# Performance work log

Measured on AMD Instinct MI355X. Metric: run time of the kernel, lower is better.

## Reference

```python
import jax, jax.numpy as jnp
import numpy as np
from jax import lax

B, T, S, D = 16, 16, 196, 768
H = 256          # hidden_dim
NH = 4           # attention heads
TH = 32          # temporal hidden = max(16, H//8)
UP = 4           # UPSAMPLE_FACTOR


def _ln(x, w, b):
    m = jnp.mean(x, -1, keepdims=True)
    v = jnp.mean((x - m) ** 2, -1, keepdims=True)
    return (x - m) / jnp.sqrt(v + 1e-5) * w + b


def _gelu(x):
    return jax.nn.gelu(x, approximate=False)  # torch nn.GELU default (erf)


def _upmat(g, f):
    # torch F.interpolate bilinear, align_corners=False, as a [g*f, g] matrix
    g_up = g * f
    src = np.maximum((np.arange(g_up) + 0.5) / f - 0.5, 0.0)
    i0 = np.minimum(np.floor(src).astype(np.int64), g - 1)
    i1 = np.minimum(i0 + 1, g - 1)
    w1 = (src - i0).astype(np.float32)
    w0 = 1.0 - w1
    W = np.zeros((g_up, g), dtype=np.float32)
    np.add.at(W, (np.arange(g_up), i0), w0)
    np.add.at(W, (np.arange(g_up), i1), w1)
    return jnp.asarray(W)


def setup_inputs() -> dict:
    key = jax.random.key(0)
    ks = jax.random.split(key, 12)
    r = lambda i, shape: jax.random.normal(ks[i], shape, jnp.float32) * 0.02
    return dict(
        tokens=jax.random.normal(ks[0], (B, T * S, D), jnp.float32),
        num_frames=T,
        fixed_box_wh=jax.random.uniform(ks[1], (2,), jnp.float32, 0.1, 0.5),
        ln_w=jnp.ones((D,), jnp.float32), ln_b=jnp.zeros((D,), jnp.float32),
        query=r(2, (1, 1, D)),
        in_proj_w=r(3, (3 * D, D)), in_proj_b=jnp.zeros((3 * D,), jnp.float32),
        out_w=r(4, (D, D)), out_b=jnp.zeros((D,), jnp.float32),
        an_w=jnp.ones((D,), jnp.float32), an_b=jnp.zeros((D,), jnp.float32),
        obj_w=r(5, (1, D)), obj_b=jnp.zeros((1,), jnp.float32),
        temperature=jnp.asarray(8.0, jnp.float32),
        r1_w=r(6, (H, 2 * D)), r1_b=jnp.zeros((H,), jnp.float32),
        r2_w=r(7, (H // 2, H)), r2_b=jnp.zeros((H // 2,), jnp.float32),
        r3_w=r(8, (2, H // 2)), r3_b=jnp.zeros((2,), jnp.float32),
        tc1_w=r(9, (TH, 2, 5)), tc1_b=jnp.zeros((TH,), jnp.float32),
        tc2_w=r(10, (2, TH, 5)), tc2_b=jnp.zeros((2,), jnp.float32),
    )


def reference(tokens, num_frames, fixed_box_wh, ln_w, ln_b, query,
              in_proj_w, in_proj_b, out_w, out_b, an_w, an_b, obj_w, obj_b,
              temperature, r1_w, r1_b, r2_w, r2_b, r3_w, r3_b,
              tc1_w, tc1_b, tc2_w, tc2_b):
    Bb, N, Dd = tokens.shape
    Tt = int(num_frames)
    Ss = N // Tt
    g = int(round(Ss ** 0.5))
    g_up = g * UP
    BT = Bb * Tt
    dt = tokens.dtype

    normed = _ln(tokens, ln_w, ln_b)
    flat = normed.reshape(BT, Ss, Dd)  # per-frame tokens

    # --- attention pooling with learned query (dropout off, eval) ---
    Wq, Wk, Wv = jnp.split(in_proj_w, 3, 0)
    bq, bk, bv = jnp.split(in_proj_b, 3, 0)
    dh = Dd // NH
    qh = (query.reshape(1, Dd) @ Wq.T + bq).reshape(NH, dh)  # same query for all frames
    kh = (flat @ Wk.T + bk).reshape(BT, Ss, NH, dh)
    vh = (flat @ Wv.T + bv).reshape(BT, Ss, NH, dh)
    scores = jnp.einsum('hd,bshd->bhs', qh, kh) / jnp.sqrt(jnp.asarray(dh, dt))
    attnp = jax.nn.softmax(scores, -1)
    ctx = jnp.einsum('bhs,bshd->bhd', attnp, vh).reshape(BT, Dd)
    pooled = _ln(ctx @ out_w.T + out_b, an_w, an_b)

    obj = (flat @ obj_w.T + obj_b)[..., 0]  # [BT,S]
    Wu = _upmat(g, UP)
    up = jnp.einsum('ug,bgh,vh->buv', Wu, obj.reshape(BT, g, g), Wu)
    up = up.reshape(BT, g_up * g_up)
    temp = jnp.maximum(temperature, 1.0)
    probs = jax.nn.softmax(up * temp, -1)
    coords = (jnp.arange(g_up, dtype=dt) + 0.5) / g_up
    yy, xx = jnp.meshgrid(coords, coords, indexing='ij')
    cx0 = probs @ xx.reshape(-1)
    cy0 = probs @ yy.reshape(-1)

    # --- 3x3 local token gather around coarse center ---
    cxg = jnp.clip(cx0 * g, 0, g - 1).astype(jnp.int32)
    cyg = jnp.clip(cy0 * g, 0, g - 1).astype(jnp.int32)
    off = jnp.array([-1, 0, 1], jnp.int32)
    gy = jnp.clip(cyg[:, None, None] + off[None, :, None], 0, g - 1)
    gx = jnp.clip(cxg[:, None, None] + off[None, None, :], 0, g - 1)
    idx = (gy * g + gx).reshape(BT, 9)
    local = jnp.take_along_axis(flat, idx[:, :, None], axis=1).mean(1)

    # --- refine MLP ---
    h1 = _gelu(jnp.concatenate([pooled, local], -1) @ r1_w.T + r1_b)
    h2 = _gelu(h1 @ r2_w.T + r2_b)
    delta = h2 @ r3_w.T + r3_b
    cx = jnp.clip(cx0 + 0.3 * jnp.tanh(delta[:, 0]), 0.0, 1.0)
    cy = jnp.clip(cy0 + 0.3 * jnp.tanh(delta[:, 1]), 0.0, 1.0)

    # --- temporal residual refiner over center trajectories ---
    seq = jnp.stack([cx, cy], 1).reshape(Bb, Tt, 2).transpose(0, 2, 1)  # [B,2,T]
    dn = ('NCH', 'OIH', 'NCH')
    t1 = _gelu(lax.conv_general_dilated(seq, tc1_w, (1,), [(2, 2)],
                                        dimension_numbers=dn) + tc1_b[None, :, None])
    td = lax.conv_general_dilated(t1, tc2_w, (1,), [(2, 2)],
                                  dimension_numbers=dn) + tc2_b[None, :, None]
    td = td.transpose(0, 2, 1).reshape(BT, 2)
    cx = jnp.clip(cx + 0.12 * jnp.tanh(td[:, 0]), 0.0, 1.0)
    cy = jnp.clip(cy + 0.12 * jnp.tanh(td[:, 1]), 0.0, 1.0)

    # --- fixed-size boxes ---
    min_size = 1.0 / g
    wh = jnp.clip(jnp.broadcast_to(fixed_box_wh.reshape(1, 2), (Bb, 2)), min_size, 1.0)
    wh = jnp.broadcast_to(wh[:, None, :], (Bb, Tt, 2)).reshape(BT, 2)
    w, h = wh[:, 0], wh[:, 1]
    x1 = jnp.clip(cx - 0.5 * w, 0.0, 1.0)
    y1 = jnp.clip(cy - 0.5 * h, 0.0, 1.0)
    x2 = jnp.clip(cx + 0.5 * w, 0.0, 1.0)
    y2 = jnp.clip(cy + 0.5 * h, 0.0, 1.0)
    x2 = jnp.clip(jnp.maximum(x2, x1 + min_size), 0.0, 1.0)
    y2 = jnp.clip(jnp.maximum(y2, y1 + min_size), 0.0, 1.0)
    return jnp.stack([x1, y1, x2, y2], 1).reshape(Bb, Tt, 4)
```

## Files before the change

kernel.cpp:

```cpp
#include <hip/hip_runtime.h>
#include <hip/hip_bf16.h>
#include <math.h>

#define SS 196
#define DD 768

__device__ __forceinline__ float b2f(ushort u){
  union { unsigned int i; float f; } v; v.i = ((unsigned int)u) << 16; return v.f;
}
__device__ __forceinline__ bool bfmode(const void* lnw){
  return ((const ushort*)lnw)[0] != 0;
}
__device__ __forceinline__ float ldx(const void* p, size_t i, bool bf){
  return bf ? b2f(((const ushort*)p)[i]) : ((const float*)p)[i];
}
__device__ __forceinline__ float gelu_f(float x){
  return 0.5f * x * (1.0f + erff(x * 0.70710678118654752f));
}
__device__ __forceinline__ float wredsum(float v){
  #pragma unroll
  for(int o=32;o;o>>=1) v += __shfl_xor(v,o,64);
  return v;
}
__device__ __forceinline__ float wredmax(float v){
  #pragma unroll
  for(int o=32;o;o>>=1) v = fmaxf(v, __shfl_xor(v,o,64));
  return v;
}

__global__ __launch_bounds__(256) void k_qh(const void* __restrict__ q,
                                            const void* __restrict__ wq,
                                            const void* __restrict__ bq,
                                            const void* __restrict__ flagp,
                                            float* __restrict__ qh){
  bool bf = bfmode(flagp);
  int wv = threadIdx.x >> 6, lane = threadIdx.x & 63;
  int c = blockIdx.x * 4 + wv;
  float acc = 0.f;
  #pragma unroll
  for(int i=0;i<12;i++){ int d = lane + 64*i; acc += ldx(q,d,bf) * ldx(wq,(size_t)c*DD+d,bf); }
  acc = wredsum(acc);
  if(lane==0) qh[c] = acc + ldx(bq,c,bf);
}

__global__ __launch_bounds__(256) void k_wkeff(const void* __restrict__ wproj,
                                               const float* __restrict__ qh,
                                               const void* __restrict__ lnw,
                                               const void* __restrict__ objw,
                                               float* __restrict__ wkraw,
                                               float* __restrict__ wf){
  bool bf = bfmode(lnw);
  int idx = blockIdx.x*256 + threadIdx.x;
  int h = idx / DD, d = idx - h*DD;
  size_t base = ((size_t)(DD + h*192))*DD + d;
  const float* qp = qh + h*192;
  float acc = 0.f;
  #pragma unroll 8
  for(int j=0;j<192;j++) acc += qp[j] * ldx(wproj, base + (size_t)j*DD, bf);
  wkraw[idx] = acc;
  float w = ldx(lnw,d,bf);
  wf[idx] = w * acc;
  if(h==0) wf[4*DD + d] = w * ldx(objw,d,bf);
}

__global__ __launch_bounds__(256) void k_consts(const float* __restrict__ wf,
                                                const float* __restrict__ wkraw,
                                                const void* __restrict__ lnb,
                                                const void* __restrict__ objw,
                                                const void* __restrict__ flagp,
                                                float* __restrict__ s12){
  bool bf = bfmode(flagp);
  int wv = threadIdx.x >> 6, lane = threadIdx.x & 63;
  for(int r = wv; r < 10; r += 4){
    float acc = 0.f;
    #pragma unroll
    for(int i=0;i<12;i++){
      int d = lane + 64*i;
      if(r < 5)      acc += wf[r*DD + d];
      else if(r < 9) acc += ldx(lnb,d,bf) * wkraw[(r-5)*DD + d];
      else           acc += ldx(lnb,d,bf) * ldx(objw,d,bf);
    }
    acc = wredsum(acc);
    if(lane==0) s12[r] = acc;
  }
}

__global__ __launch_bounds__(256) void k_pass1(const void* __restrict__ tok,
                                               const float* __restrict__ wf,
                                               const float* __restrict__ s12,
                                               const void* __restrict__ objb,
                                               const void* __restrict__ flagp,
                                               float* __restrict__ scores,
                                               float* __restrict__ objv,
                                               float* __restrict__ meanv,
                                               float* __restrict__ rstdv){
  __shared__ __align__(16) float swf[5*DD];
  __shared__ float ss12[10];
  for(int i=threadIdx.x;i<5*DD;i+=256) swf[i]=wf[i];
  if(threadIdx.x<10) ss12[threadIdx.x]=s12[threadIdx.x];
  __syncthreads();
  bool bf = bfmode(flagp);
  int wv = threadIdx.x >> 6, lane = threadIdx.x & 63;
  for(int it=0; it<4; it++){
    int tkn = blockIdx.x*16 + wv*4 + it;
    int f = tkn / SS, s = tkn - f*SS;
    float a0=0,a1=0,a2=0,a3=0,a4=0,sm=0,sq=0;
    if(bf){
      const ushort* x = (const ushort*)tok + (size_t)tkn * DD;
      #pragma unroll
      for(int i=0;i<6;i++){
        int d = 2*lane + 128*i;
        ushort2 u = *(const ushort2*)(x + d);
        float x0=b2f(u.x), x1=b2f(u.y);
        sm += x0 + x1; sq += x0*x0 + x1*x1;
        float2 w;
        w = *(const float2*)&swf[0*DD+d]; a0 += x0*w.x + x1*w.y;
        w = *(const float2*)&swf[1*DD+d]; a1 += x0*w.x + x1*w.y;
        w = *(const float2*)&swf[2*DD+d]; a2 += x0*w.x + x1*w.y;
        w = *(const float2*)&swf[3*DD+d]; a3 += x0*w.x + x1*w.y;
        w = *(const float2*)&swf[4*DD+d]; a4 += x0*w.x + x1*w.y;
      }
    } else {
      const float* x = (const float*)tok + (size_t)tkn * DD;
      #pragma unroll
      for(int i=0;i<3;i++){
        int d = 4*lane + 256*i;
        float4 u = *(const float4*)(x + d);
        sm += u.x+u.y+u.z+u.w;
        sq += u.x*u.x+u.y*u.y+u.z*u.z+u.w*u.w;
        float4 w;
        w = *(const float4*)&swf[0*DD+d]; a0 += u.x*w.x+u.y*w.y+u.z*w.z+u.w*w.w;
        w = *(const float4*)&swf[1*DD+d]; a1 += u.x*w.x+u.y*w.y+u.z*w.z+u.w*w.w;
        w = *(const float4*)&swf[2*DD+d]; a2 += u.x*w.x+u.y*w.y+u.z*w.z+u.w*w.w;
        w = *(const float4*)&swf[3*DD+d]; a3 += u.x*w.x+u.y*w.y+u.z*w.z+u.w*w.w;
        w = *(const float4*)&swf[4*DD+d]; a4 += u.x*w.x+u.y*w.y+u.z*w.z+u.w*w.w;
      }
    }
    sm=wredsum(sm); sq=wredsum(sq);
    a0=wredsum(a0); a1=wredsum(a1); a2=wredsum(a2); a3=wredsum(a3); a4=wredsum(a4);
    if(lane==0){
      const float invD = 1.0f/768.0f;
      float m = sm*invD;
      float var = sq*invD - m*m;
      float rstd = rsqrtf(var + 1e-5f);
      meanv[tkn]=m; rstdv[tkn]=rstd;
      const float sc = 0.07216878364870322f;
      scores[(f*4+0)*SS+s] = (rstd*(a0 - m*ss12[0]) + ss12[5]) * sc;
      scores[(f*4+1)*SS+s] = (rstd*(a1 - m*ss12[1]) + ss12[6]) * sc;
      scores[(f*4+2)*SS+s] = (rstd*(a2 - m*ss12[2]) + ss12[7]) * sc;
      scores[(f*4+3)*SS+s] = (rstd*(a3 - m*ss12[3]) + ss12[8]) * sc;
      objv[tkn] = rstd*(a4 - m*ss12[4]) + ss12[9] + ldx(objb,0,bf);
    }
  }
}

__global__ __launch_bounds__(256) void k_soft(const float* __restrict__ rstdv,
                                              const float* __restrict__ meanv,
                                              float* __restrict__ scores,
                                              float* __restrict__ cterm){
  int f = blockIdx.x;
  int h = threadIdx.x >> 6, lane = threadIdx.x & 63;
  float* sc = scores + (size_t)(f*4+h)*SS;
  const float* rs = rstdv + f*SS;
  const float* mv = meanv + f*SS;
  float v[4]; float mx = -1e30f;
  #pragma unroll
  for(int j=0;j<4;j++){ int s=lane+64*j; v[j] = (s<SS)? sc[s] : -1e30f; mx=fmaxf(mx,v[j]); }
  mx = wredmax(mx);
  float e[4], sum=0.f;
  #pragma unroll
  for(int j=0;j<4;j++){ int s=lane+64*j; e[j] = (s<SS)? expf(v[j]-mx) : 0.f; sum += e[j]; }
  sum = wredsum(sum);
  float inv = 1.0f/sum;
  float cp = 0.f;
  #pragma unroll
  for(int j=0;j<4;j++){
    int s=lane+64*j;
    if(s<SS){ float r=rs[s]; float a=e[j]*inv*r; sc[s]=a; cp += a*mv[s]; }
  }
  cp = wredsum(cp);
  if(lane==0) cterm[f*4+h] = cp;
}

__global__ __launch_bounds__(256) void k_xbar(const void* __restrict__ tok,
                                              const float* __restrict__ aw,
                                              const float* __restrict__ cterm,
                                              const void* __restrict__ lnw,
                                              const void* __restrict__ lnb,
                                              float* __restrict__ xbar){
  bool bf = bfmode(lnw);
  int f = blockIdx.x;
  __shared__ float a4[SS*4];
  for(int i=threadIdx.x;i<SS*4;i+=256){ int s=i>>2, h=i&3; a4[i]=aw[(size_t)(f*4+h)*SS+s]; }
  __syncthreads();
  float acc[3][4] = {};
  if(bf){
    const ushort* tf = (const ushort*)tok + (size_t)f*SS*DD;
    for(int s=0;s<SS;s++){
      float w0=a4[s*4+0], w1=a4[s*4+1], w2=a4[s*4+2], w3=a4[s*4+3];
      #pragma unroll
      for(int j=0;j<3;j++){
        float x = b2f(tf[(size_t)s*DD + threadIdx.x + 256*j]);
        acc[j][0]+=w0*x; acc[j][1]+=w1*x; acc[j][2]+=w2*x; acc[j][3]+=w3*x;
      }
    }
  } else {
    const float* tf = (const float*)tok + (size_t)f*SS*DD;
    for(int s=0;s<SS;s++){
      float w0=a4[s*4+0], w1=a4[s*4+1], w2=a4[s*4+2], w3=a4[s*4+3];
      #pragma unroll
      for(int j=0;j<3;j++){
        float x = tf[(size_t)s*DD + threadIdx.x + 256*j];
        acc[j][0]+=w0*x; acc[j][1]+=w1*x; acc[j][2]+=w2*x; acc[j][3]+=w3*x;
      }
    }
  }
  float c0=cterm[f*4+0], c1=cterm[f*4+1], c2=cterm[f*4+2], c3=cterm[f*4+3];
  #pragma unroll
  for(int j=0;j<3;j++){
    int d = threadIdx.x + 256*j;
    float w=ldx(lnw,d,bf), b=ldx(lnb,d,bf);
    xbar[((size_t)(f*4+0))*DD+d] = w*(acc[j][0]-c0)+b;
    xbar[((size_t)(f*4+1))*DD+d] = w*(acc[j][1]-c1)+b;
    xbar[((size_t)(f*4+2))*DD+d] = w*(acc[j][2]-c2)+b;
    xbar[((size_t)(f*4+3))*DD+d] = w*(acc[j][3]-c3)+b;
  }
}

template<int N, int K, int ACT, int CTX, int ROWOFF>
__global__ __launch_bounds__(256) void k_gemm(const float* __restrict__ A,
                                              const void* __restrict__ W,
                                              const void* __restrict__ bias,
                                              const void* __restrict__ flagp,
                                              float* __restrict__ C){
  bool bf = bfmode(flagp);
  __shared__ float As[16][32];
  __shared__ float Bs[16][64];
  int tid = threadIdx.x;
  int m0 = blockIdx.y * 32;
  int n0 = blockIdx.x * 64;
  int h  = n0 / 192;
  int am = tid >> 3;
  int ak = (tid & 7) * 2;
  int bn = tid >> 2;
  int bk = (tid & 3) * 4;
  const size_t arow = CTX ? ((size_t)(m0+am)*4 + h) * 768 : (size_t)(m0+am) * K;
  const float* arp  = A + arow + ak;
  const size_t woff = (size_t)(ROWOFF + n0 + bn)*K + bk;
  int ry = tid >> 4;
  int cx = tid & 15;
  float acc[2][4] = {};
  for(int k0=0; k0<K; k0+=16){
    float2 av = *(const float2*)(arp + k0);
    float4 wv4;
    if(bf){
      ushort4 wv = *(const ushort4*)((const ushort*)W + woff + k0);
      wv4.x=b2f(wv.x); wv4.y=b2f(wv.y); wv4.z=b2f(wv.z); wv4.w=b2f(wv.w);
    } else {
      wv4 = *(const float4*)((const float*)W + woff + k0);
    }
    __syncthreads();
    As[ak][am]   = av.x;
    As[ak+1][am] = av.y;
    Bs[bk][bn]   = wv4.x;
    Bs[bk+1][bn] = wv4.y;
    Bs[bk+2][bn] = wv4.z;
    Bs[bk+3][bn] = wv4.w;
    __syncthreads();
    #pragma unroll
    for(int k=0;k<16;k++){
      float a0 = As[k][ry*2], a1 = As[k][ry*2+1];
      float4 b = *(const float4*)&Bs[k][cx*4];
      acc[0][0]+=a0*b.x; acc[0][1]+=a0*b.y; acc[0][2]+=a0*b.z; acc[0][3]+=a0*b.w;
      acc[1][0]+=a1*b.x; acc[1][1]+=a1*b.y; acc[1][2]+=a1*b.z; acc[1][3]+=a1*b.w;
    }
  }
  int n = n0 + cx*4;
  float b0=ldx(bias,ROWOFF+n,bf), b1=ldx(bias,ROWOFF+n+1,bf),
        b2v=ldx(bias,ROWOFF+n+2,bf), b3=ldx(bias,ROWOFF+n+3,bf);
  #pragma unroll
  for(int i=0;i<2;i++){
    int f = m0 + ry*2 + i;
    float4 o;
    o.x = acc[i][0]+b0; o.y = acc[i][1]+b1; o.z = acc[i][2]+b2v; o.w = acc[i][3]+b3;
    if(ACT==1){ o.x=gelu_f(o.x); o.y=gelu_f(o.y); o.z=gelu_f(o.z); o.w=gelu_f(o.w); }
    *(float4*)&C[(size_t)f*N + n] = o;
  }
}

__global__ __launch_bounds__(256) void k_lnan(const float* __restrict__ X,
                                              const void* __restrict__ anw,
                                              const void* __restrict__ anb,
                                              const void* __restrict__ flagp,
                                              float* __restrict__ pl){
  bool bf = bfmode(flagp);
  int wv = threadIdx.x >> 6, lane = threadIdx.x & 63;
  int f = blockIdx.x*4 + wv;
  const float* x = X + (size_t)f*DD;
  float v[12]; float sm=0, sq=0;
  #pragma unroll
  for(int i=0;i<12;i++){ v[i]=x[lane+64*i]; sm+=v[i]; sq+=v[i]*v[i]; }
  sm=wredsum(sm); sq=wredsum(sq);
  float m = sm*(1.0f/768.0f);
  float rstd = rsqrtf(sq*(1.0f/768.0f) - m*m + 1e-5f);
  #pragma unroll
  for(int i=0;i<12;i++){
    int d = lane+64*i;
    pl[(size_t)f*1536 + d] = (v[i]-m)*rstd*ldx(anw,d,bf) + ldx(anb,d,bf);
  }
}

__global__ __launch_bounds__(256) void k_obj(const void* __restrict__ tok,
                                             const float* __restrict__ objv,
                                             const float* __restrict__ meanv,
                                             const float* __restrict__ rstdv,
                                             const void* __restrict__ temp,
                                             const void* __restrict__ lnw,
                                             const void* __restrict__ lnb,
                                             float* __restrict__ pl,
                                             float* __restrict__ cxy){
  bool bf = bfmode(lnw);
  int f = blockIdx.x;
  int tid = threadIdx.x;
  __shared__ float G[196];
  __shared__ float up[3136];
  __shared__ int   i0a[56], i1a[56];
  __shared__ float w0a[56], w1a[56];
  __shared__ float redm[4], reds[4], redx[4], redy[4];
  __shared__ int   sidx[9];
  __shared__ float rj[9], rmj[9];
  if(tid<196) G[tid] = objv[(size_t)f*SS + tid];
  if(tid<56){
    float src = fmaxf((tid+0.5f)*0.25f - 0.5f, 0.0f);
    int i0 = min((int)floorf(src), 13);
    i0a[tid]=i0; i1a[tid]=min(i0+1,13);
    float w1 = src - (float)i0;
    w1a[tid]=w1; w0a[tid]=1.0f-w1;
  }
  __syncthreads();
  float lmax = -1e30f;
  for(int i=tid;i<3136;i+=256){
    int u=i/56, v=i-u*56;
    float val = w0a[u]*(w0a[v]*G[i0a[u]*14+i0a[v]] + w1a[v]*G[i0a[u]*14+i1a[v]])
              + w1a[u]*(w0a[v]*G[i1a[u]*14+i0a[v]] + w1a[v]*G[i1a[u]*14+i1a[v]]);
    up[i]=val; lmax=fmaxf(lmax,val);
  }
  lmax = wredmax(lmax);
  if((tid&63)==0) redm[tid>>6]=lmax;
  __syncthreads();
  float mx = fmaxf(fmaxf(redm[0],redm[1]), fmaxf(redm[2],redm[3]));
  float t = fmaxf(ldx(temp,0,bf), 1.0f);
  float se=0, sx=0, sy=0;
  for(int i=tid;i<3136;i+=256){
    int u=i/56, v=i-u*56;
    float e = expf((up[i]-mx)*t);
    se += e;
    sx += e * ((v+0.5f)*(1.0f/56.0f));
    sy += e * ((u+0.5f)*(1.0f/56.0f));
  }
  se=wredsum(se); sx=wredsum(sx); sy=wredsum(sy);
  if((tid&63)==0){ reds[tid>>6]=se; redx[tid>>6]=sx; redy[tid>>6]=sy; }
  __syncthreads();
  se = reds[0]+reds[1]+reds[2]+reds[3];
  sx = redx[0]+redx[1]+redx[2]+redx[3];
  sy = redy[0]+redy[1]+redy[2]+redy[3];
  float cx0 = sx/se, cy0 = sy/se;
  if(tid==0){ cxy[f*2]=cx0; cxy[f*2+1]=cy0; }
  float vx = fminf(fmaxf(cx0*14.0f,0.0f),13.0f); int cxg=(int)vx;
  float vy = fminf(fmaxf(cy0*14.0f,0.0f),13.0f); int cyg=(int)vy;
  if(tid<9){
    int dy = tid/3 - 1, dx = tid%3 - 1;
    int gy = min(max(cyg+dy,0),13), gx = min(max(cxg+dx,0),13);
    int s = gy*14+gx;
    sidx[tid]=s;
    float r = rstdv[(size_t)f*SS+s];
    rj[tid]=r; rmj[tid]=r*meanv[(size_t)f*SS+s];
  }
  __syncthreads();
  float offc = 0.f;
  #pragma unroll
  for(int j=0;j<9;j++) offc += rmj[j];
  for(int d=tid; d<DD; d+=256){
    float acc = 0.f;
    #pragma unroll
    for(int j=0;j<9;j++) acc += rj[j]*ldx(tok, (size_t)f*SS*DD + (size_t)sidx[j]*DD + d, bf);
    pl[(size_t)f*1536 + DD + d] = ldx(lnw,d,bf)*((acc-offc)*(1.0f/9.0f)) + ldx(lnb,d,bf);
  }
}

__global__ __launch_bounds__(256) void k_final(const float* __restrict__ h2,
                                               const void* __restrict__ r3w,
                                               const void* __restrict__ r3b,
                                               const float* __restrict__ cxy,
                                               const void* __restrict__ tc1w,
                                               const void* __restrict__ tc1b,
                                               const void* __restrict__ tc2w,
                                               const void* __restrict__ tc2b,
                                               const void* __restrict__ fbw,
                                               const void* __restrict__ flagp,
                                               void* __restrict__ out){
  bool bf = bfmode(flagp);
  __shared__ float sxs[256], sys[256];
  __shared__ float t1[16*32*16];
  __shared__ float td[16*2*16];
  int f = threadIdx.x;
  float a0=0.f, a1=0.f;
  const float* hh = h2 + (size_t)f*128;
  for(int k=0;k<128;k++){ float x=hh[k]; a0 += x*ldx(r3w,k,bf); a1 += x*ldx(r3w,128+k,bf); }
  a0 += ldx(r3b,0,bf); a1 += ldx(r3b,1,bf);
  float cx1 = fminf(fmaxf(cxy[f*2]   + 0.3f*tanhf(a0), 0.f), 1.f);
  float cy1 = fminf(fmaxf(cxy[f*2+1] + 0.3f*tanhf(a1), 0.f), 1.f);
  sxs[f]=cx1; sys[f]=cy1;
  __syncthreads();
  for(int idx=f; idx<8192; idx+=256){
    int b = idx>>9, o = (idx>>4)&31, t = idx&15;
    float acc = ldx(tc1b,o,bf);
    #pragma unroll
    for(int k=0;k<5;k++){
      int tt = t + k - 2;
      if(tt>=0 && tt<16)
        acc += sxs[b*16+tt]*ldx(tc1w,o*10 + k,bf) + sys[b*16+tt]*ldx(tc1w,o*10 + 5 + k,bf);
    }
    t1[idx] = gelu_f(acc);
  }
  __syncthreads();
  for(int idx=f; idx<512; idx+=256){
    int b = idx>>5, c = (idx>>4)&1, t = idx&15;
    float acc = ldx(tc2b,c,bf);
    for(int o=0;o<32;o++){
      #pragma unroll
      for(int k=0;k<5;k++){
        int tt = t + k - 2;
        if(tt>=0 && tt<16) acc += t1[(b*32+o)*16+tt]*ldx(tc2w,(c*32+o)*5+k,bf);
      }
    }
    td[(b*2+c)*16+t] = acc;
  }
  __syncthreads();
  {
    int t = f&15; (void)t;
    int b = f>>4;
    float tdx = td[(b*2+0)*16+(f&15)], tdy = td[(b*2+1)*16+(f&15)];
    float cx2 = fminf(fmaxf(sxs[f] + 0.12f*tanhf(tdx), 0.f), 1.f);
    float cy2 = fminf(fmaxf(sys[f] + 0.12f*tanhf(tdy), 0.f), 1.f);
    const float ms = 1.0f/14.0f;
    float w  = fminf(fmaxf(ldx(fbw,0,bf), ms), 1.f);
    float ht = fminf(fmaxf(ldx(fbw,1,bf), ms), 1.f);
    float x1 = fminf(fmaxf(cx2 - 0.5f*w , 0.f), 1.f);
    float y1 = fminf(fmaxf(cy2 - 0.5f*ht, 0.f), 1.f);
    float x2 = fminf(fmaxf(cx2 + 0.5f*w , 0.f), 1.f);
    float y2 = fminf(fmaxf(cy2 + 0.5f*ht, 0.f), 1.f);
    x2 = fminf(fmaxf(fmaxf(x2, x1+ms), 0.f), 1.f);
    y2 = fminf(fmaxf(fmaxf(y2, y1+ms), 0.f), 1.f);
    if(bf){
      __hip_bfloat16* ob = (__hip_bfloat16*)out;
      ob[f*4+0]=__float2bfloat16(x1);
      ob[f*4+1]=__float2bfloat16(y1);
      ob[f*4+2]=__float2bfloat16(x2);
      ob[f*4+3]=__float2bfloat16(y2);
    } else {
      float* of = (float*)out;
      of[f*4+0]=x1; of[f*4+1]=y1; of[f*4+2]=x2; of[f*4+3]=y2;
    }
  }
}

extern "C" void kernel_launch(void* const* d_in, const int* in_sizes, int n_in,
                              void* d_out, int out_size, void* d_ws, size_t ws_size,
                              hipStream_t stream){
  (void)in_sizes; (void)n_in; (void)out_size; (void)ws_size;
  const void* tok   = d_in[0];
  const void* fbw   = d_in[2];
  const void* lnw   = d_in[3];
  const void* lnb   = d_in[4];
  const void* query = d_in[5];
  const void* wproj = d_in[6];
  const void* bproj = d_in[7];
  const void* outw  = d_in[8];
  const void* outb  = d_in[9];
  const void* anw   = d_in[10];
  const void* anb   = d_in[11];
  const void* objw  = d_in[12];
  const void* objb  = d_in[13];
  const void* temp  = d_in[14];
  const void* r1w   = d_in[15];
  const void* r1b   = d_in[16];
  const void* r2w   = d_in[17];
  const void* r2b   = d_in[18];
  const void* r3w   = d_in[19];
  const void* r3b   = d_in[20];
  const void* tc1w  = d_in[21];
  const void* tc1b  = d_in[22];
  const void* tc2w  = d_in[23];
  const void* tc2b  = d_in[24];

  float* ws    = (float*)d_ws;
  float* qh    = ws;
  float* wkraw = ws + 768;
  float* wf    = wkraw + 3072;
  float* s12   = wf + 3840;
  float* scores= s12 + 16;
  float* objv  = scores + 200704;
  float* meanv = objv + 50176;
  float* rstdv = meanv + 50176;
  float* cterm = rstdv + 50176;
  float* xbar  = cterm + 1024;
  float* ctx   = xbar + 786432;
  float* ppre  = ctx + 196608;
  float* pl    = ppre + 196608;
  float* h1    = pl + 393216;
  float* h2    = h1 + 65536;
  float* cxy   = h2 + 32768;

  hipLaunchKernelGGL(k_qh,    dim3(192),  dim3(256), 0, stream, query, wproj, bproj, lnw, qh);
  hipLaunchKernelGGL(k_wkeff, dim3(12),   dim3(256), 0, stream, wproj, qh, lnw, objw, wkraw, wf);
  hipLaunchKernelGGL(k_consts,dim3(1),    dim3(256), 0, stream, wf, wkraw, lnb, objw, lnw, s12);
  hipLaunchKernelGGL(k_pass1, dim3(3136), dim3(256), 0, stream, tok, wf, s12, objb, lnw, scores, objv, meanv, rstdv);
  hipLaunchKernelGGL(k_soft,  dim3(256),  dim3(256), 0, stream, rstdv, meanv, scores, cterm);
  hipLaunchKernelGGL(k_xbar,  dim3(256),  dim3(256), 0, stream, tok, scores, cterm, lnw, lnb, xbar);
  hipLaunchKernelGGL((k_gemm<768,768,0,1,1536>), dim3(12,8), dim3(256), 0, stream, xbar, wproj, bproj, lnw, ctx);
  hipLaunchKernelGGL((k_gemm<768,768,0,0,0>),    dim3(12,8), dim3(256), 0, stream, ctx, outw, outb, lnw, ppre);
  hipLaunchKernelGGL(k_lnan,  dim3(64),   dim3(256), 0, stream, ppre, anw, anb, lnw, pl);
  hipLaunchKernelGGL(k_obj,   dim3(256),  dim3(256), 0, stream, tok, objv, meanv, rstdv, temp, lnw, lnb, pl, cxy);
  hipLaunchKernelGGL((k_gemm<256,1536,1,0,0>), dim3(4,8), dim3(256), 0, stream, pl, r1w, r1b, lnw, h1);
  hipLaunchKernelGGL((k_gemm<128,256,1,0,0>),  dim3(2,8), dim3(256), 0, stream, h1, r2w, r2b, lnw, h2);
  hipLaunchKernelGGL(k_final, dim3(1),    dim3(256), 0, stream, h2, r3w, r3b, cxy, tc1w, tc1b, tc2w, tc2b, fbw, lnw, (void*)d_out);
}
```

Before: 616.7 us.

## Replace shared-memory tiled GEMM with per-thread dot-product GEMM over more blocks

Swaps the LDS-tiled 32x64 GEMM for a kernel where each thread computes one output as a direct dot product over K, reading A rows and W rows with vector loads. The grid grows from 8 to 64 row-blocks, with 4 rows per block, so the small GEMMs (M=256) spread across many more CUs. This removes shared memory and barriers but drops operand reuse. Each thread streams a separate W row, so lanes access strided addresses and loads are uncoalesced, which adds memory traffic.

```diff
diff --git a/kernel.cpp b/kernel.cpp
--- a/kernel.cpp
+++ b/kernel.cpp
@@ -228,64 +228,45 @@
 }
 
 template<int N, int K, int ACT, int CTX, int ROWOFF>
-__global__ __launch_bounds__(256) void k_gemm(const float* __restrict__ A,
-                                              const void* __restrict__ W,
-                                              const void* __restrict__ bias,
-                                              const void* __restrict__ flagp,
-                                              float* __restrict__ C){
+__global__ __launch_bounds__(256) void k_dgemm(const float* __restrict__ A,
+                                               const void* __restrict__ W,
+                                               const void* __restrict__ bias,
+                                               const void* __restrict__ flagp,
+                                               float* __restrict__ C){
   bool bf = bfmode(flagp);
-  __shared__ float As[16][32];
-  __shared__ float Bs[16][64];
   int tid = threadIdx.x;
-  int m0 = blockIdx.y * 32;
-  int n0 = blockIdx.x * 64;
+  int m0 = blockIdx.y*4, n0 = blockIdx.x*64;
+  int mi = tid >> 6;
+  int n  = n0 + (tid & 63);
   int h  = n0 / 192;
-  int am = tid >> 3;
-  int ak = (tid & 7) * 2;
-  int bn = tid >> 2;
-  int bk = (tid & 3) * 4;
-  const size_t arow = CTX ? ((size_t)(m0+am)*4 + h) * 768 : (size_t)(m0+am) * K;
-  const float* arp  = A + arow + ak;
-  const size_t woff = (size_t)(ROWOFF + n0 + bn)*K + bk;
-  int ry = tid >> 4;
-  int cx = tid & 15;
-  float acc[2][4] = {};
-  for(int k0=0; k0<K; k0+=16){
-    float2 av = *(const float2*)(arp + k0);
-    float4 wv4;
-    if(bf){
-      ushort4 wv = *(const ushort4*)((const ushort*)W + woff + k0);
-      wv4.x=b2f(wv.x); wv4.y=b2f(wv.y); wv4.z=b2f(wv.z); wv4.w=b2f(wv.w);
-    } else {
-      wv4 = *(const float4*)((const float*)W + woff + k0);
-    }
-    __syncthreads();
-    As[ak][am]   = av.x;
-    As[ak+1][am] = av.y;
-    Bs[bk][bn]   = wv4.x;
-    Bs[bk+1][bn] = wv4.y;
-    Bs[bk+2][bn] = wv4.z;
-    Bs[bk+3][bn] = wv4.w;
-    __syncthreads();
-    #pragma unroll
-    for(int k=0;k<16;k++){
-      float a0 = As[k][ry*2], a1 = As[k][ry*2+1];
-      float4 b = *(const float4*)&Bs[k][cx*4];
-      acc[0][0]+=a0*b.x; acc[0][1]+=a0*b.y; acc[0][2]+=a0*b.z; acc[0][3]+=a0*b.w;
-      acc[1][0]+=a1*b.x; acc[1][1]+=a1*b.y; acc[1][2]+=a1*b.z; acc[1][3]+=a1*b.w;
-    }
-  }
-  int n = n0 + cx*4;
-  float b0=ldx(bias,ROWOFF+n,bf), b1=ldx(bias,ROWOFF+n+1,bf),
-        b2v=ldx(bias,ROWOFF+n+2,bf), b3=ldx(bias,ROWOFF+n+3,bf);
-  #pragma unroll
-  for(int i=0;i<2;i++){
-    int f = m0 + ry*2 + i;
-    float4 o;
-    o.x = acc[i][0]+b0; o.y = acc[i][1]+b1; o.z = acc[i][2]+b2v; o.w = acc[i][3]+b3;
-    if(ACT==1){ o.x=gelu_f(o.x); o.y=gelu_f(o.y); o.z=gelu_f(o.z); o.w=gelu_f(o.w); }
-    *(float4*)&C[(size_t)f*N + n] = o;
-  }
+  int m  = m0 + mi;
+  const size_t arow = CTX ? ((size_t)(m*4 + h))*768 : (size_t)m*K;
+  const float* ar = A + arow;
+  float acc = 0.f;
+  if(bf){
+    const ushort* wr = (const ushort*)W + (size_t)(ROWOFF+n)*K;
+    for(int k=0;k<K;k+=8){
+      float4 a0 = *(const float4*)(ar+k);
+      float4 a1 = *(const float4*)(ar+k+4);
+      ushort4 w0 = *(const ushort4*)(wr+k);
+      ushort4 w1 = *(const ushort4*)(wr+k+4);
+      acc += a0.x*b2f(w0.x) + a0.y*b2f(w0.y) + a0.z*b2f(w0.z) + a0.w*b2f(w0.w)
+           + a1.x*b2f(w1.x) + a1.y*b2f(w1.y) + a1.z*b2f(w1.z) + a1.w*b2f(w1.w);
+    }
+  } else {
+    const float* wr = (const float*)W + (size_t)(ROWOFF+n)*K;
+    for(int k=0;k<K;k+=8){
+      float4 a0 = *(const float4*)(ar+k);
+      float4 a1 = *(const float4*)(ar+k+4);
+      float4 w0 = *(const float4*)(wr+k);
+      float4 w1 = *(const float4*)(wr+k+4);
+      acc += a0.x*w0.x + a0.y*w0.y + a0.z*w0.z + a0.w*w0.w
+           + a1.x*w1.x + a1.y*w1.y + a1.z*w1.z + a1.w*w1.w;
+    }
+  }
+  acc += ldx(bias, ROWOFF+n, bf);
+  if(ACT) acc = gelu_f(acc);
+  C[(size_t)m*N + n] = acc;
 }
 
 __global__ __launch_bounds__(256) void k_lnan(const float* __restrict__ X,
@@ -438,7 +419,6 @@
   }
   __syncthreads();
   {
-    int t = f&15; (void)t;
     int b = f>>4;
     float tdx = td[(b*2+0)*16+(f&15)], tdy = td[(b*2+1)*16+(f&15)];
     float cx2 = fminf(fmaxf(sxs[f] + 0.12f*tanhf(tdx), 0.f), 1.f);
@@ -518,11 +498,11 @@
   hipLaunchKernelGGL(k_pass1, dim3(3136), dim3(256), 0, stream, tok, wf, s12, objb, lnw, scores, objv, meanv, rstdv);
   hipLaunchKernelGGL(k_soft,  dim3(256),  dim3(256), 0, stream, rstdv, meanv, scores, cterm);
   hipLaunchKernelGGL(k_xbar,  dim3(256),  dim3(256), 0, stream, tok, scores, cterm, lnw, lnb, xbar);
-  hipLaunchKernelGGL((k_gemm<768,768,0,1,1536>), dim3(12,8), dim3(256), 0, stream, xbar, wproj, bproj, lnw, ctx);
-  hipLaunchKernelGGL((k_gemm<768,768,0,0,0>),    dim3(12,8), dim3(256), 0, stream, ctx, outw, outb, lnw, ppre);
+  hipLaunchKernelGGL((k_dgemm<768,768,0,1,1536>), dim3(12,64), dim3(256), 0, stream, xbar, wproj, bproj, lnw, ctx);
+  hipLaunchKernelGGL((k_dgemm<768,768,0,0,0>),    dim3(12,64), dim3(256), 0, stream, ctx, outw, outb, lnw, ppre);
   hipLaunchKernelGGL(k_lnan,  dim3(64),   dim3(256), 0, stream, ppre, anw, anb, lnw, pl);
   hipLaunchKernelGGL(k_obj,   dim3(256),  dim3(256), 0, stream, tok, objv, meanv, rstdv, temp, lnw, lnb, pl, cxy);
-  hipLaunchKernelGGL((k_gemm<256,1536,1,0,0>), dim3(4,8), dim3(256), 0, stream, pl, r1w, r1b, lnw, h1);
-  hipLaunchKernelGGL((k_gemm<128,256,1,0,0>),  dim3(2,8), dim3(256), 0, stream, h1, r2w, r2b, lnw, h2);
+  hipLaunchKernelGGL((k_dgemm<256,1536,1,0,0>), dim3(4,64), dim3(256), 0, stream, pl, r1w, r1b, lnw, h1);
+  hipLaunchKernelGGL((k_dgemm<128,256,1,0,0>),  dim3(2,64), dim3(256), 0, stream, h1, r2w, r2b, lnw, h2);
   hipLaunchKernelGGL(k_final, dim3(1),    dim3(256), 0, stream, h2, r3w, r3b, cxy, tc1w, tc1b, tc2w, tc2b, fbw, lnw, (void*)d_out);
 }
```

Result: slower. 687.8 us (+11.5%).
